# Optimization experiments

Hardware: AMD Instinct MI355X
Metric: run time of the kernel (lower is better)

Reference implementation:

```python
import jax, jax.numpy as jnp
import numpy as np

# Model constants (match init_kwargs)
NUM_HEADS = 8
IN_BITS = 64
N_STATE = 256
N_OUT = 64
K_CONN = 8            # n_bits_per_output_neuron
HASH = 65536          # hash_size
K_BITS = 3            # routing key bits
B = 128               # batch of independent sequences
T = 128               # timesteps (windows) per sequence


def setup_inputs() -> dict:
    key = jax.random.key(0)
    k1, k2, k3, k4, k5, k6 = jax.random.split(key, 6)
    # flat bit sequences, split into T windows of IN_BITS in reference()
    bits = jax.random.randint(k1, (B, T * IN_BITS), 0, 2, dtype=jnp.int32)
    # state layer: full connectivity (default n_bits_per_state_neuron =
    # input_bits + n_state_neurons), hashed addressing via random odd-ish
    # integer coefficients dotted with the bit vector, mod HASH.
    total_in = IN_BITS + N_STATE  # 320
    state_coeffs = jax.random.randint(k2, (N_STATE, total_in), 1, HASH, dtype=jnp.int32)
    state_mem = jax.random.uniform(k3, (N_STATE, HASH), dtype=jnp.float32)
    # output heads: each neuron connects to K_CONN random state bits
    head_conn = jax.random.randint(k4, (NUM_HEADS, N_OUT, K_CONN), 0, N_STATE, dtype=jnp.int32)
    head_coeffs = jax.random.randint(k5, (NUM_HEADS, N_OUT, K_CONN), 1, HASH, dtype=jnp.int32)
    head_mem = jax.random.uniform(k6, (NUM_HEADS, N_OUT, HASH), dtype=jnp.float32)
    return {
        "bits": bits,
        "state_coeffs": state_coeffs,
        "state_mem": state_mem,
        "head_conn": head_conn,
        "head_coeffs": head_coeffs,
        "head_mem": head_mem,
    }


def reference(bits, state_coeffs, state_mem, head_conn, head_coeffs, head_mem):
    # windows: [B, T, IN_BITS]
    windows = bits.reshape(B, T, IN_BITS)
    n_state, hash_size = state_mem.shape

    def step(state, w):  # state: [B, N_STATE] int32 bits; w: [B, IN_BITS]
        x = jnp.concatenate([w, state], axis=1)                 # [B, IN+N]
        addr = (x @ state_coeffs.T) % hash_size                 # hashed address [B, N]
        vals = state_mem[jnp.arange(n_state), addr]             # gather [B, N]
        new_state = (vals >= 0.5).astype(jnp.int32)             # RAM output bits
        return new_state, None

    state0 = jnp.zeros((B, n_state), jnp.int32)
    final_state, _ = jax.lax.scan(step, state0, jnp.swapaxes(windows, 0, 1))

    # all output heads read the shared final state
    sel = final_state[:, head_conn]                             # [B, H, O, K]
    addr_h = jnp.einsum('bhok,hok->bho', sel, head_coeffs) % hash_size
    head_vals = head_mem[jnp.arange(NUM_HEADS)[:, None],
                         jnp.arange(N_OUT)[None, :], addr_h]    # [B, H, O]

    # kv routing: pack last K_BITS bits of the final window (MSB first)
    last_w = windows[:, -1, :]
    pow2 = 2 ** jnp.arange(K_BITS - 1, -1, -1)
    head_idx = jnp.sum(last_w[:, -K_BITS:] * pow2, axis=1) % NUM_HEADS  # [B]

    out = head_vals[jnp.arange(B), head_idx]                    # [B, N_OUT]
    return out
```

## Files before the change

kernel.cpp:

```cpp
#include <hip/hip_runtime.h>
#include <stdint.h>

#define T_ 128

typedef int v4i __attribute__((ext_vector_type(4)));

__global__ void prep_bfrag(const int* __restrict__ sc, uint4* __restrict__ bf) {
  int gid = blockIdx.x * 256 + threadIdx.x;
  if (gid >= 160 * 64) return;
  int mf = gid >> 6, l = gid & 63;
  int tau = mf / 10, rem = mf % 10;
  int kap = rem >> 1, h = rem & 1;
  int j = 16 * tau + (l & 15);
  int kinb = (l >> 4) * 16;
  unsigned wout[4];
#pragma unroll
  for (int r = 0; r < 4; ++r) {
    unsigned wrd = 0;
#pragma unroll
    for (int be = 0; be < 4; ++be) {
      int kin = kinb + 4 * r + be;
      int col = (kap == 0) ? kin : 64 + ((kap - 1) << 6) + kin;
      unsigned c = (unsigned)sc[j * 320 + col];
      unsigned byte = (h ? (c >> 8) : c) & 0xFFu;
      byte = (byte - 128u) & 0xFFu;
      wrd |= byte << (8 * be);
    }
    wout[r] = wrd;
  }
  bf[gid] = make_uint4(wout[0], wout[1], wout[2], wout[3]);
}

__global__ void prep_wbits(const int* __restrict__ bits,
                           unsigned long long* __restrict__ wb) {
  int gid = blockIdx.x * 256 + threadIdx.x;
  int wv = gid >> 6, lane = gid & 63;
  unsigned long long m = __ballot(bits[gid] != 0);
  if (lane == 0) wb[wv] = m;
}

__global__ void prep_bitpack(const float* __restrict__ sm,
                             unsigned long long* __restrict__ packed) {
  int base = blockIdx.x * (256 * 32) + threadIdx.x;
  int lane = threadIdx.x & 63;
#pragma unroll 1
  for (int it = 0; it < 32; ++it) {
    int idx = base + it * 256;
    float v = sm[idx];
    unsigned long long m = __ballot(v >= 0.5f);
    if (lane == 0) packed[idx >> 6] = m;
  }
}

static __device__ __forceinline__ v4i expand16(unsigned b16) {
  v4i a;
#pragma unroll
  for (int r = 0; r < 4; ++r) {
    unsigned nib = (b16 >> (4 * r)) & 0xFu;
    a[r] = (int)((nib * 0x00204081u) & 0x01010101u);
  }
  return a;
}

__global__ __launch_bounds__(256, 1) void scan_heads(
    const uint4* __restrict__ bfrag,
    const unsigned long long* __restrict__ wbits,
    const unsigned* __restrict__ packed32,
    const int* __restrict__ head_conn,
    const int* __restrict__ head_coeffs,
    const float* __restrict__ head_mem,
    float* __restrict__ out) {
  __shared__ __align__(16) unsigned char ab[2][256];
  __shared__ __align__(16) unsigned mcnt[2][4];
  const int tid = threadIdx.x;
  const int b = blockIdx.x;
  const int w = tid >> 6, l = tid & 63;
  const int qq = l >> 4;
  const int j = 64 * w + l;

  v4i bf[4][5][2];
#pragma unroll
  for (int i = 0; i < 4; ++i)
#pragma unroll
    for (int k = 0; k < 5; ++k)
#pragma unroll
      for (int h = 0; h < 2; ++h) {
        int mf = ((4 * w + i) * 5 + k) * 2 + h;
        bf[i][k][h] = __builtin_bit_cast(v4i, bfrag[mf * 64 + l]);
      }

  ab[0][tid] = (unsigned char)0;
  if (tid < 4) mcnt[0][tid] = 0u;

  unsigned long long wcur = wbits[b * 128];
  const unsigned* pkrow = packed32 + ((size_t)j << 11);

  v4i acc[4][2];
  {
    v4i aw = expand16((unsigned)((wcur >> (16 * qq)) & 0xFFFFu));
    v4i z = (v4i){0, 0, 0, 0};
#pragma unroll
    for (int i = 0; i < 4; ++i)
#pragma unroll
      for (int h = 0; h < 2; ++h)
        acc[i][h] = __builtin_amdgcn_mfma_i32_16x16x64_i8(aw, bf[i][0][h], z, 0, 0, 0);
  }
  __syncthreads();

  int cur = 0;
#pragma unroll 1
  for (int t = 0; t < T_; ++t) {
    int tn = (t + 1 < T_) ? t + 1 : t;
    unsigned long long wnext = wbits[b * 128 + tn];

    uint4 cz = *((const uint4*)&mcnt[cur][0]);
    unsigned NB = cz.x + cz.y + cz.z + cz.w + (unsigned)__popcll(wcur);

#pragma unroll
    for (int c = 0; c < 4; ++c) {
      v4i a = *((const v4i*)&ab[cur][64 * c + 16 * qq]);
      acc[0][0] = __builtin_amdgcn_mfma_i32_16x16x64_i8(a, bf[0][c + 1][0], acc[0][0], 0, 0, 0);
      acc[0][1] = __builtin_amdgcn_mfma_i32_16x16x64_i8(a, bf[0][c + 1][1], acc[0][1], 0, 0, 0);
      acc[1][0] = __builtin_amdgcn_mfma_i32_16x16x64_i8(a, bf[1][c + 1][0], acc[1][0], 0, 0, 0);
      acc[1][1] = __builtin_amdgcn_mfma_i32_16x16x64_i8(a, bf[1][c + 1][1], acc[1][1], 0, 0, 0);
      acc[2][0] = __builtin_amdgcn_mfma_i32_16x16x64_i8(a, bf[2][c + 1][0], acc[2][0], 0, 0, 0);
      acc[2][1] = __builtin_amdgcn_mfma_i32_16x16x64_i8(a, bf[2][c + 1][1], acc[2][1], 0, 0, 0);
      acc[3][0] = __builtin_amdgcn_mfma_i32_16x16x64_i8(a, bf[3][c + 1][0], acc[3][0], 0, 0, 0);
      acc[3][1] = __builtin_amdgcn_mfma_i32_16x16x64_i8(a, bf[3][c + 1][1], acc[3][1], 0, 0, 0);
    }

    unsigned corr = (NB * 32896u) & 0xFFFFu;
    unsigned lo01 = (l & 16) ? (unsigned)acc[1][0][0] : (unsigned)acc[0][0][0];
    unsigned lo23 = (l & 16) ? (unsigned)acc[3][0][0] : (unsigned)acc[2][0][0];
    unsigned hi01 = (l & 16) ? (unsigned)acc[1][1][0] : (unsigned)acc[0][1][0];
    unsigned hi23 = (l & 16) ? (unsigned)acc[3][1][0] : (unsigned)acc[2][1][0];
    unsigned lo = (l & 32) ? lo23 : lo01;
    unsigned hi = (l & 32) ? hi23 : hi01;
    unsigned ad = (lo + (hi << 8) + corr) & 0xFFFFu;

    unsigned word = pkrow[ad >> 5];

    {
      v4i aw = expand16((unsigned)((wnext >> (16 * qq)) & 0xFFFFu));
      v4i z = (v4i){0, 0, 0, 0};
#pragma unroll
      for (int i = 0; i < 4; ++i)
#pragma unroll
        for (int h = 0; h < 2; ++h)
          acc[i][h] = __builtin_amdgcn_mfma_i32_16x16x64_i8(aw, bf[i][0][h], z, 0, 0, 0);
    }

    unsigned bitv = (word >> (ad & 31)) & 1u;
    unsigned long long mq = __ballot(bitv != 0u);
    int nxt = cur ^ 1;
    ab[nxt][j] = (unsigned char)bitv;
    if (l == 0) mcnt[nxt][w] = (unsigned)__popcll(mq);

    __syncthreads();
    cur = nxt;
    wcur = wnext;
  }

  if (w == 0) {
    int h = (int)((((wcur >> 61) & 1) << 2) | (((wcur >> 62) & 1) << 1) |
                  ((wcur >> 63) & 1));
    int ho = h * 64 + l;
    const int4* cn4 = (const int4*)(head_conn + ho * 8);
    const int4* cf4 = (const int4*)(head_coeffs + ho * 8);
    int4 cna = cn4[0], cnb = cn4[1];
    int4 cfa = cf4[0], cfb = cf4[1];
    int cns[8] = {cna.x, cna.y, cna.z, cna.w, cnb.x, cnb.y, cnb.z, cnb.w};
    int cfs[8] = {cfa.x, cfa.y, cfa.z, cfa.w, cfb.x, cfb.y, cfb.z, cfb.w};
    unsigned addr = 0;
#pragma unroll
    for (int k = 0; k < 8; ++k) {
      addr += (unsigned)ab[cur][cns[k]] * (unsigned)cfs[k];
    }
    addr &= 0xFFFFu;
    out[b * 64 + l] = head_mem[((size_t)ho << 16) + addr];
  }
}

extern "C" void kernel_launch(void* const* d_in, const int* in_sizes, int n_in,
                              void* d_out, int out_size, void* d_ws, size_t ws_size,
                              hipStream_t stream) {
  const int*   bits         = (const int*)d_in[0];
  const int*   state_coeffs = (const int*)d_in[1];
  const float* state_mem    = (const float*)d_in[2];
  const int*   head_conn    = (const int*)d_in[3];
  const int*   head_coeffs  = (const int*)d_in[4];
  const float* head_mem     = (const float*)d_in[5];
  float* out = (float*)d_out;

  char* ws = (char*)d_ws;
  uint4*              bfrag  = (uint4*)ws;
  unsigned long long* wbits  = (unsigned long long*)(ws + (160 << 10));
  unsigned*           packed = (unsigned*)(ws + (288 << 10));

  prep_bfrag<<<40, 256, 0, stream>>>(state_coeffs, bfrag);
  prep_wbits<<<4096, 256, 0, stream>>>(bits, wbits);
  prep_bitpack<<<2048, 256, 0, stream>>>(state_mem, (unsigned long long*)packed);
  scan_heads<<<128, 256, 0, stream>>>(bfrag, wbits, packed,
                                      head_conn, head_coeffs, head_mem, out);
}
```

Baseline: 324.1 us.

## Precompute window hash contributions in a separate GEMM kernel and split recurrent MFMA chains

Adds a prep kernel that computes each timestep's window-input contribution to the hashed addresses, including the popcount correction, for all batches and timesteps up front, and stores them as 16-bit values. The scan loop then only does the state-dependent MFMAs and adds the precomputed value, with the per-wave count pre-multiplied by the correction constant. The eight dependent MFMAs per output tile are split into two independent accumulator chains to shorten the serial dependency. The barrier is replaced with an explicit waitcnt and s_barrier, and the loop is unrolled by two. This adds an extra kernel launch and a workspace buffer in exchange for a shorter per-step critical path in the recurrent loop.

Result: slower. 333.6 us (+2.9%).

```diff
diff --git a/kernel.cpp b/kernel.cpp
--- a/kernel.cpp
+++ b/kernel.cpp
@@ -62,10 +62,38 @@
   return a;
 }
 
+__global__ void prep_wgemm(const uint4* __restrict__ bfrag,
+                           const unsigned long long* __restrict__ wb,
+                           unsigned short* __restrict__ win) {
+  int wave = blockIdx.x * 4 + (threadIdx.x >> 6);
+  int l = threadIdx.x & 63;
+  int qq = l >> 4;
+  v4i z = (v4i){0, 0, 0, 0};
+#pragma unroll 1
+  for (int mi = 0; mi < 4; ++mi) {
+    int m = wave * 4 + mi;
+    unsigned long long wrow = wb[m];
+    v4i aw = expand16((unsigned)((wrow >> (16 * qq)) & 0xFFFFu));
+    unsigned corr = (unsigned)__popcll(wrow) * 32896u;
+#pragma unroll 1
+    for (int tau = 0; tau < 16; ++tau) {
+      v4i blo = __builtin_bit_cast(v4i, bfrag[(tau * 10 + 0) * 64 + l]);
+      v4i bhi = __builtin_bit_cast(v4i, bfrag[(tau * 10 + 1) * 64 + l]);
+      v4i alo = __builtin_amdgcn_mfma_i32_16x16x64_i8(aw, blo, z, 0, 0, 0);
+      v4i ahi = __builtin_amdgcn_mfma_i32_16x16x64_i8(aw, bhi, z, 0, 0, 0);
+      if (l < 16) {
+        unsigned ad = ((unsigned)alo[0] + ((unsigned)ahi[0] << 8) + corr) & 0xFFFFu;
+        win[(size_t)m * 256 + tau * 16 + l] = (unsigned short)ad;
+      }
+    }
+  }
+}
+
 __global__ __launch_bounds__(256, 1) void scan_heads(
     const uint4* __restrict__ bfrag,
+    const unsigned short* __restrict__ win,
+    const unsigned* __restrict__ packed32,
     const unsigned long long* __restrict__ wbits,
-    const unsigned* __restrict__ packed32,
     const int* __restrict__ head_conn,
     const int* __restrict__ head_coeffs,
     const float* __restrict__ head_mem,
@@ -78,92 +106,86 @@
   const int qq = l >> 4;
   const int j = 64 * w + l;
 
-  v4i bf[4][5][2];
+  v4i bf[4][4][2];
 #pragma unroll
   for (int i = 0; i < 4; ++i)
 #pragma unroll
-    for (int k = 0; k < 5; ++k)
+    for (int c = 0; c < 4; ++c)
 #pragma unroll
       for (int h = 0; h < 2; ++h) {
-        int mf = ((4 * w + i) * 5 + k) * 2 + h;
-        bf[i][k][h] = __builtin_bit_cast(v4i, bfrag[mf * 64 + l]);
+        int mf = ((4 * w + i) * 5 + (c + 1)) * 2 + h;
+        bf[i][c][h] = __builtin_bit_cast(v4i, bfrag[mf * 64 + l]);
       }
 
   ab[0][tid] = (unsigned char)0;
   if (tid < 4) mcnt[0][tid] = 0u;
 
-  unsigned long long wcur = wbits[b * 128];
   const unsigned* pkrow = packed32 + ((size_t)j << 11);
-
-  v4i acc[4][2];
-  {
-    v4i aw = expand16((unsigned)((wcur >> (16 * qq)) & 0xFFFFu));
+  unsigned vw = (unsigned)win[(size_t)(b * 128) * 256 + j];
+  __syncthreads();
+
+#pragma unroll 2
+  for (int t = 0; t < T_; ++t) {
+    const int cur = t & 1, nxt = cur ^ 1;
+
+    const unsigned char* abase = &ab[cur][16 * qq];
+    v4i a0 = *(const v4i*)(abase);
+    v4i a1 = *(const v4i*)(abase + 64);
+    v4i a2 = *(const v4i*)(abase + 128);
+    v4i a3 = *(const v4i*)(abase + 192);
+    uint4 cz = *((const uint4*)&mcnt[cur][0]);
+
+    int tn = (t + 1 < T_) ? t + 1 : t;
+    unsigned vwn = (unsigned)win[(size_t)(b * 128 + tn) * 256 + j];
+
     v4i z = (v4i){0, 0, 0, 0};
-#pragma unroll
-    for (int i = 0; i < 4; ++i)
-#pragma unroll
-      for (int h = 0; h < 2; ++h)
-        acc[i][h] = __builtin_amdgcn_mfma_i32_16x16x64_i8(aw, bf[i][0][h], z, 0, 0, 0);
-  }
-  __syncthreads();
-
-  int cur = 0;
-#pragma unroll 1
-  for (int t = 0; t < T_; ++t) {
-    int tn = (t + 1 < T_) ? t + 1 : t;
-    unsigned long long wnext = wbits[b * 128 + tn];
-
-    uint4 cz = *((const uint4*)&mcnt[cur][0]);
-    unsigned NB = cz.x + cz.y + cz.z + cz.w + (unsigned)__popcll(wcur);
-
-#pragma unroll
-    for (int c = 0; c < 4; ++c) {
-      v4i a = *((const v4i*)&ab[cur][64 * c + 16 * qq]);
-      acc[0][0] = __builtin_amdgcn_mfma_i32_16x16x64_i8(a, bf[0][c + 1][0], acc[0][0], 0, 0, 0);
-      acc[0][1] = __builtin_amdgcn_mfma_i32_16x16x64_i8(a, bf[0][c + 1][1], acc[0][1], 0, 0, 0);
-      acc[1][0] = __builtin_amdgcn_mfma_i32_16x16x64_i8(a, bf[1][c + 1][0], acc[1][0], 0, 0, 0);
-      acc[1][1] = __builtin_amdgcn_mfma_i32_16x16x64_i8(a, bf[1][c + 1][1], acc[1][1], 0, 0, 0);
-      acc[2][0] = __builtin_amdgcn_mfma_i32_16x16x64_i8(a, bf[2][c + 1][0], acc[2][0], 0, 0, 0);
-      acc[2][1] = __builtin_amdgcn_mfma_i32_16x16x64_i8(a, bf[2][c + 1][1], acc[2][1], 0, 0, 0);
-      acc[3][0] = __builtin_amdgcn_mfma_i32_16x16x64_i8(a, bf[3][c + 1][0], acc[3][0], 0, 0, 0);
-      acc[3][1] = __builtin_amdgcn_mfma_i32_16x16x64_i8(a, bf[3][c + 1][1], acc[3][1], 0, 0, 0);
-    }
-
-    unsigned corr = (NB * 32896u) & 0xFFFFu;
-    unsigned lo01 = (l & 16) ? (unsigned)acc[1][0][0] : (unsigned)acc[0][0][0];
-    unsigned lo23 = (l & 16) ? (unsigned)acc[3][0][0] : (unsigned)acc[2][0][0];
-    unsigned hi01 = (l & 16) ? (unsigned)acc[1][1][0] : (unsigned)acc[0][1][0];
-    unsigned hi23 = (l & 16) ? (unsigned)acc[3][1][0] : (unsigned)acc[2][1][0];
-    unsigned lo = (l & 32) ? lo23 : lo01;
-    unsigned hi = (l & 32) ? hi23 : hi01;
-    unsigned ad = (lo + (hi << 8) + corr) & 0xFFFFu;
+    v4i accA[4][2], accB[4][2];
+#pragma unroll
+    for (int i = 0; i < 4; ++i) {
+      accA[i][0] = __builtin_amdgcn_mfma_i32_16x16x64_i8(a0, bf[i][0][0], z, 0, 0, 0);
+      accA[i][1] = __builtin_amdgcn_mfma_i32_16x16x64_i8(a0, bf[i][0][1], z, 0, 0, 0);
+      accB[i][0] = __builtin_amdgcn_mfma_i32_16x16x64_i8(a2, bf[i][2][0], z, 0, 0, 0);
+      accB[i][1] = __builtin_amdgcn_mfma_i32_16x16x64_i8(a2, bf[i][2][1], z, 0, 0, 0);
+    }
+#pragma unroll
+    for (int i = 0; i < 4; ++i) {
+      accA[i][0] = __builtin_amdgcn_mfma_i32_16x16x64_i8(a1, bf[i][1][0], accA[i][0], 0, 0, 0);
+      accA[i][1] = __builtin_amdgcn_mfma_i32_16x16x64_i8(a1, bf[i][1][1], accA[i][1], 0, 0, 0);
+      accB[i][0] = __builtin_amdgcn_mfma_i32_16x16x64_i8(a3, bf[i][3][0], accB[i][0], 0, 0, 0);
+      accB[i][1] = __builtin_amdgcn_mfma_i32_16x16x64_i8(a3, bf[i][3][1], accB[i][1], 0, 0, 0);
+    }
+
+    unsigned csum = cz.x + cz.y + cz.z + cz.w;
+    unsigned loA = (l & 16) ? (unsigned)accA[1][0][0] : (unsigned)accA[0][0][0];
+    unsigned loA2 = (l & 16) ? (unsigned)accA[3][0][0] : (unsigned)accA[2][0][0];
+    unsigned hiA = (l & 16) ? (unsigned)accA[1][1][0] : (unsigned)accA[0][1][0];
+    unsigned hiA2 = (l & 16) ? (unsigned)accA[3][1][0] : (unsigned)accA[2][1][0];
+    unsigned loB = (l & 16) ? (unsigned)accB[1][0][0] : (unsigned)accB[0][0][0];
+    unsigned loB2 = (l & 16) ? (unsigned)accB[3][0][0] : (unsigned)accB[2][0][0];
+    unsigned hiB = (l & 16) ? (unsigned)accB[1][1][0] : (unsigned)accB[0][1][0];
+    unsigned hiB2 = (l & 16) ? (unsigned)accB[3][1][0] : (unsigned)accB[2][1][0];
+    unsigned lo = ((l & 32) ? loA2 : loA) + ((l & 32) ? loB2 : loB);
+    unsigned hi = ((l & 32) ? hiA2 : hiA) + ((l & 32) ? hiB2 : hiB);
+    unsigned ad = (lo + (hi << 8) + csum + vw) & 0xFFFFu;
 
     unsigned word = pkrow[ad >> 5];
-
-    {
-      v4i aw = expand16((unsigned)((wnext >> (16 * qq)) & 0xFFFFu));
-      v4i z = (v4i){0, 0, 0, 0};
-#pragma unroll
-      for (int i = 0; i < 4; ++i)
-#pragma unroll
-        for (int h = 0; h < 2; ++h)
-          acc[i][h] = __builtin_amdgcn_mfma_i32_16x16x64_i8(aw, bf[i][0][h], z, 0, 0, 0);
-    }
-
     unsigned bitv = (word >> (ad & 31)) & 1u;
     unsigned long long mq = __ballot(bitv != 0u);
-    int nxt = cur ^ 1;
     ab[nxt][j] = (unsigned char)bitv;
-    if (l == 0) mcnt[nxt][w] = (unsigned)__popcll(mq);
-
-    __syncthreads();
-    cur = nxt;
-    wcur = wnext;
+    if (l == 0) mcnt[nxt][w] = (unsigned)__popcll(mq) * 32896u;
+
+    asm volatile("s_waitcnt lgkmcnt(0)" ::: "memory");
+    __builtin_amdgcn_sched_barrier(0);
+    __builtin_amdgcn_s_barrier();
+    __builtin_amdgcn_sched_barrier(0);
+
+    vw = vwn;
   }
 
   if (w == 0) {
-    int h = (int)((((wcur >> 61) & 1) << 2) | (((wcur >> 62) & 1) << 1) |
-                  ((wcur >> 63) & 1));
+    unsigned long long wl = wbits[b * 128 + 127];
+    int h = (int)((((wl >> 61) & 1) << 2) | (((wl >> 62) & 1) << 1) |
+                  ((wl >> 63) & 1));
     int ho = h * 64 + l;
     const int4* cn4 = (const int4*)(head_conn + ho * 8);
     const int4* cf4 = (const int4*)(head_coeffs + ho * 8);
@@ -174,7 +196,7 @@
     unsigned addr = 0;
 #pragma unroll
     for (int k = 0; k < 8; ++k) {
-      addr += (unsigned)ab[cur][cns[k]] * (unsigned)cfs[k];
+      addr += (unsigned)ab[T_ & 1][cns[k]] * (unsigned)cfs[k];
     }
     addr &= 0xFFFFu;
     out[b * 64 + l] = head_mem[((size_t)ho << 16) + addr];
@@ -196,10 +218,12 @@
   uint4*              bfrag  = (uint4*)ws;
   unsigned long long* wbits  = (unsigned long long*)(ws + (160 << 10));
   unsigned*           packed = (unsigned*)(ws + (288 << 10));
+  unsigned short*     win    = (unsigned short*)(ws + (288 << 10) + (2 << 20));
 
   prep_bfrag<<<40, 256, 0, stream>>>(state_coeffs, bfrag);
   prep_wbits<<<4096, 256, 0, stream>>>(bits, wbits);
   prep_bitpack<<<2048, 256, 0, stream>>>(state_mem, (unsigned long long*)packed);
-  scan_heads<<<128, 256, 0, stream>>>(bfrag, wbits, packed,
+  prep_wgemm<<<1024, 256, 0, stream>>>(bfrag, wbits, win);
+  scan_heads<<<128, 256, 0, stream>>>(bfrag, win, packed, wbits,
                                       head_conn, head_coeffs, head_mem, out);
 }
```

## Split MFMA accumulation into two independent chains and pipeline window term

Applied to the files above, without the earlier changes.

Splits the serial chain of four dependent MFMAs per accumulator into two parallel chains (A and B) that are summed at the end, cutting the MFMA dependency latency on the per-timestep critical path. The window-bit MFMA for the next step now goes into a double-buffered accumulator with a precomputed popcount correction, and the per-warp count correction is premultiplied when written. The loop is unrolled by two with compile-time buffer indices, and __syncthreads is replaced by an explicit lgkmcnt wait plus s_barrier fenced by sched_barriers. This uses more registers for the extra accumulators and the hand-placed barrier relies on the waitcnt to keep LDS ordering correct.

Measured after the change: 319.8 us. About the same (-1.3%).

```diff
diff --git a/kernel.cpp b/kernel.cpp
--- a/kernel.cpp
+++ b/kernel.cpp
@@ -64,8 +64,8 @@
 
 __global__ __launch_bounds__(256, 1) void scan_heads(
     const uint4* __restrict__ bfrag,
+    const unsigned* __restrict__ packed32,
     const unsigned long long* __restrict__ wbits,
-    const unsigned* __restrict__ packed32,
     const int* __restrict__ head_conn,
     const int* __restrict__ head_coeffs,
     const float* __restrict__ head_mem,
@@ -92,10 +92,11 @@
   ab[0][tid] = (unsigned char)0;
   if (tid < 4) mcnt[0][tid] = 0u;
 
+  const unsigned* pkrow = packed32 + ((size_t)j << 11);
   unsigned long long wcur = wbits[b * 128];
-  const unsigned* pkrow = packed32 + ((size_t)j << 11);
-
-  v4i acc[4][2];
+
+  v4i wacc[2][4][2];
+  unsigned wcorr[2];
   {
     v4i aw = expand16((unsigned)((wcur >> (16 * qq)) & 0xFFFFu));
     v4i z = (v4i){0, 0, 0, 0};
@@ -103,61 +104,77 @@
     for (int i = 0; i < 4; ++i)
 #pragma unroll
       for (int h = 0; h < 2; ++h)
-        acc[i][h] = __builtin_amdgcn_mfma_i32_16x16x64_i8(aw, bf[i][0][h], z, 0, 0, 0);
+        wacc[0][i][h] = __builtin_amdgcn_mfma_i32_16x16x64_i8(aw, bf[i][0][h], z, 0, 0, 0);
+    wcorr[0] = (unsigned)__popcll(wcur) * 32896u;
   }
   __syncthreads();
 
-  int cur = 0;
-#pragma unroll 1
+#pragma unroll 2
   for (int t = 0; t < T_; ++t) {
+    const int cur = t & 1, nxt = cur ^ 1;
+
     int tn = (t + 1 < T_) ? t + 1 : t;
     unsigned long long wnext = wbits[b * 128 + tn];
 
+    const unsigned char* abase = &ab[cur][16 * qq];
+    v4i a0 = *(const v4i*)(abase);
+    v4i a1 = *(const v4i*)(abase + 64);
+    v4i a2 = *(const v4i*)(abase + 128);
+    v4i a3 = *(const v4i*)(abase + 192);
     uint4 cz = *((const uint4*)&mcnt[cur][0]);
-    unsigned NB = cz.x + cz.y + cz.z + cz.w + (unsigned)__popcll(wcur);
-
-#pragma unroll
-    for (int c = 0; c < 4; ++c) {
-      v4i a = *((const v4i*)&ab[cur][64 * c + 16 * qq]);
-      acc[0][0] = __builtin_amdgcn_mfma_i32_16x16x64_i8(a, bf[0][c + 1][0], acc[0][0], 0, 0, 0);
-      acc[0][1] = __builtin_amdgcn_mfma_i32_16x16x64_i8(a, bf[0][c + 1][1], acc[0][1], 0, 0, 0);
-      acc[1][0] = __builtin_amdgcn_mfma_i32_16x16x64_i8(a, bf[1][c + 1][0], acc[1][0], 0, 0, 0);
-      acc[1][1] = __builtin_amdgcn_mfma_i32_16x16x64_i8(a, bf[1][c + 1][1], acc[1][1], 0, 0, 0);
-      acc[2][0] = __builtin_amdgcn_mfma_i32_16x16x64_i8(a, bf[2][c + 1][0], acc[2][0], 0, 0, 0);
-      acc[2][1] = __builtin_amdgcn_mfma_i32_16x16x64_i8(a, bf[2][c + 1][1], acc[2][1], 0, 0, 0);
-      acc[3][0] = __builtin_amdgcn_mfma_i32_16x16x64_i8(a, bf[3][c + 1][0], acc[3][0], 0, 0, 0);
-      acc[3][1] = __builtin_amdgcn_mfma_i32_16x16x64_i8(a, bf[3][c + 1][1], acc[3][1], 0, 0, 0);
-    }
-
-    unsigned corr = (NB * 32896u) & 0xFFFFu;
-    unsigned lo01 = (l & 16) ? (unsigned)acc[1][0][0] : (unsigned)acc[0][0][0];
-    unsigned lo23 = (l & 16) ? (unsigned)acc[3][0][0] : (unsigned)acc[2][0][0];
-    unsigned hi01 = (l & 16) ? (unsigned)acc[1][1][0] : (unsigned)acc[0][1][0];
-    unsigned hi23 = (l & 16) ? (unsigned)acc[3][1][0] : (unsigned)acc[2][1][0];
-    unsigned lo = (l & 32) ? lo23 : lo01;
-    unsigned hi = (l & 32) ? hi23 : hi01;
-    unsigned ad = (lo + (hi << 8) + corr) & 0xFFFFu;
+
+    v4i z = (v4i){0, 0, 0, 0};
+    v4i accA[4][2], accB[4][2];
+#pragma unroll
+    for (int i = 0; i < 4; ++i) {
+      accA[i][0] = __builtin_amdgcn_mfma_i32_16x16x64_i8(a0, bf[i][1][0], wacc[cur][i][0], 0, 0, 0);
+      accA[i][1] = __builtin_amdgcn_mfma_i32_16x16x64_i8(a0, bf[i][1][1], wacc[cur][i][1], 0, 0, 0);
+      accB[i][0] = __builtin_amdgcn_mfma_i32_16x16x64_i8(a2, bf[i][3][0], z, 0, 0, 0);
+      accB[i][1] = __builtin_amdgcn_mfma_i32_16x16x64_i8(a2, bf[i][3][1], z, 0, 0, 0);
+    }
+#pragma unroll
+    for (int i = 0; i < 4; ++i) {
+      accA[i][0] = __builtin_amdgcn_mfma_i32_16x16x64_i8(a1, bf[i][2][0], accA[i][0], 0, 0, 0);
+      accA[i][1] = __builtin_amdgcn_mfma_i32_16x16x64_i8(a1, bf[i][2][1], accA[i][1], 0, 0, 0);
+      accB[i][0] = __builtin_amdgcn_mfma_i32_16x16x64_i8(a3, bf[i][4][0], accB[i][0], 0, 0, 0);
+      accB[i][1] = __builtin_amdgcn_mfma_i32_16x16x64_i8(a3, bf[i][4][1], accB[i][1], 0, 0, 0);
+    }
+
+    unsigned csum = cz.x + cz.y + cz.z + cz.w + wcorr[cur];
+    unsigned tv0 = ((unsigned)accA[0][0][0] + (unsigned)accB[0][0][0]) +
+                   (((unsigned)accA[0][1][0] + (unsigned)accB[0][1][0]) << 8);
+    unsigned tv1 = ((unsigned)accA[1][0][0] + (unsigned)accB[1][0][0]) +
+                   (((unsigned)accA[1][1][0] + (unsigned)accB[1][1][0]) << 8);
+    unsigned tv2 = ((unsigned)accA[2][0][0] + (unsigned)accB[2][0][0]) +
+                   (((unsigned)accA[2][1][0] + (unsigned)accB[2][1][0]) << 8);
+    unsigned tv3 = ((unsigned)accA[3][0][0] + (unsigned)accB[3][0][0]) +
+                   (((unsigned)accA[3][1][0] + (unsigned)accB[3][1][0]) << 8);
+    unsigned t01 = (l & 16) ? tv1 : tv0;
+    unsigned t23 = (l & 16) ? tv3 : tv2;
+    unsigned ad = (((l & 32) ? t23 : t01) + csum) & 0xFFFFu;
 
     unsigned word = pkrow[ad >> 5];
 
     {
       v4i aw = expand16((unsigned)((wnext >> (16 * qq)) & 0xFFFFu));
-      v4i z = (v4i){0, 0, 0, 0};
 #pragma unroll
       for (int i = 0; i < 4; ++i)
 #pragma unroll
         for (int h = 0; h < 2; ++h)
-          acc[i][h] = __builtin_amdgcn_mfma_i32_16x16x64_i8(aw, bf[i][0][h], z, 0, 0, 0);
+          wacc[nxt][i][h] = __builtin_amdgcn_mfma_i32_16x16x64_i8(aw, bf[i][0][h], z, 0, 0, 0);
+      wcorr[nxt] = (unsigned)__popcll(wnext) * 32896u;
     }
 
     unsigned bitv = (word >> (ad & 31)) & 1u;
     unsigned long long mq = __ballot(bitv != 0u);
-    int nxt = cur ^ 1;
     ab[nxt][j] = (unsigned char)bitv;
-    if (l == 0) mcnt[nxt][w] = (unsigned)__popcll(mq);
-
-    __syncthreads();
-    cur = nxt;
+    if (l == 0) mcnt[nxt][w] = (unsigned)__popcll(mq) * 32896u;
+
+    asm volatile("s_waitcnt lgkmcnt(0)" ::: "memory");
+    __builtin_amdgcn_sched_barrier(0);
+    __builtin_amdgcn_s_barrier();
+    __builtin_amdgcn_sched_barrier(0);
+
     wcur = wnext;
   }
 
@@ -174,7 +191,7 @@
     unsigned addr = 0;
 #pragma unroll
     for (int k = 0; k < 8; ++k) {
-      addr += (unsigned)ab[cur][cns[k]] * (unsigned)cfs[k];
+      addr += (unsigned)ab[T_ & 1][cns[k]] * (unsigned)cfs[k];
     }
     addr &= 0xFFFFu;
     out[b * 64 + l] = head_mem[((size_t)ho << 16) + addr];
@@ -200,6 +217,6 @@
   prep_bfrag<<<40, 256, 0, stream>>>(state_coeffs, bfrag);
   prep_wbits<<<4096, 256, 0, stream>>>(bits, wbits);
   prep_bitpack<<<2048, 256, 0, stream>>>(state_mem, (unsigned long long*)packed);
-  scan_heads<<<128, 256, 0, stream>>>(bfrag, wbits, packed,
+  scan_heads<<<128, 256, 0, stream>>>(bfrag, packed, wbits,
                                       head_conn, head_coeffs, head_mem, out);
 }
```
